# Performance work log

Measured on AMD Instinct MI355X. Metric: run time of the kernel, lower is better.

Reference implementation:

```python
import jax, jax.numpy as jnp
import numpy as np

N, E, IN_CH, H, L = 100000, 1600000, 64, 128, 4
BN_EPS = 1e-5

def setup_inputs() -> dict:
    key = jax.random.key(0)
    ks = jax.random.split(key, 20)
    s = 0.1
    return {
        'x': jax.random.normal(ks[0], (N, IN_CH), jnp.float32),
        'edge_index': jax.random.randint(ks[1], (2, E), 0, N, jnp.int64),
        'W_in': jax.random.normal(ks[2], (H, IN_CH), jnp.float32) * s,
        'b_in': jnp.zeros((H,), jnp.float32),
        'msg_W1': jax.random.normal(ks[3], (L, H, H), jnp.float32) * s,
        'msg_b1': jnp.zeros((L, H), jnp.float32),
        'msg_W2': jax.random.normal(ks[4], (L, H, H), jnp.float32) * s,
        'msg_b2': jnp.zeros((L, H), jnp.float32),
        'gru_Wih': jax.random.normal(ks[5], (L, 3 * H, H), jnp.float32) * s,
        'gru_bih': jnp.zeros((L, 3 * H), jnp.float32),
        'gru_Whh': jax.random.normal(ks[6], (L, 3 * H, H), jnp.float32) * s,
        'gru_bhh': jnp.zeros((L, 3 * H), jnp.float32),
        'bn_gamma': jnp.ones((L, H), jnp.float32),
        'bn_beta': jnp.zeros((L, H), jnp.float32),
        'W_out': jax.random.normal(ks[7], (1, H), jnp.float32) * s,
        'b_out': jnp.zeros((1,), jnp.float32),
    }

def reference(x, edge_index, W_in, b_in, msg_W1, msg_b1, msg_W2, msg_b2,
              gru_Wih, gru_bih, gru_Whh, gru_bhh, bn_gamma, bn_beta, W_out, b_out):
    n = x.shape[0]
    src, dst = edge_index[0], edge_index[1]  # j (source), i (target)
    h = jax.nn.relu(x @ W_in.T + b_in)  # [N, H]
    for l in range(L):
        residual = h
        # message: MLP on gathered source features (dropout off, eval mode)
        xj = h[src]  # [E, H] gather
        m = jax.nn.relu(xj @ msg_W1[l].T + msg_b1[l]) @ msg_W2[l].T + msg_b2[l]
        # aggregate: scatter-add into target nodes
        aggr = jax.ops.segment_sum(m, dst, num_segments=n)  # [N, H]
        # GRUCell update: input=aggr, hidden=h
        gi = aggr @ gru_Wih[l].T + gru_bih[l]  # [N, 3H]
        gh = h @ gru_Whh[l].T + gru_bhh[l]     # [N, 3H]
        i_r, i_z, i_n = jnp.split(gi, 3, axis=-1)
        h_r, h_z, h_n = jnp.split(gh, 3, axis=-1)
        r = jax.nn.sigmoid(i_r + h_r)
        z = jax.nn.sigmoid(i_z + h_z)
        ng = jnp.tanh(i_n + r * h_n)
        h = (1.0 - z) * ng + z * h
        # BatchNorm over node dim (batch statistics) + residual
        mu = jnp.mean(h, axis=0)
        var = jnp.mean((h - mu) ** 2, axis=0)
        h = bn_gamma[l] * (h - mu) * jax.lax.rsqrt(var + BN_EPS) + bn_beta[l]
        h = h + residual
    out = h @ W_out.T + b_out  # [N, 1]
    return out.squeeze(-1)
```

## Files before the change

### kernel.cpp

```cpp
#include <hip/hip_runtime.h>
#include <hip/hip_bf16.h>

#define NN 100000
#define EE 1600000
#define HH 128
#define LL 4
#define BN_EPS 1e-5f
#define NPART 6252
#define SCAN_BLK 391

typedef __attribute__((ext_vector_type(8))) short bf16x8;
typedef __attribute__((ext_vector_type(4))) float f32x4;
typedef unsigned short u16;

static __device__ __forceinline__ u16 f2bf(float f) {
  unsigned u = __float_as_uint(f);
  u += 0x7FFF + ((u >> 16) & 1);
  return (u16)(u >> 16);
}
static __device__ __forceinline__ float bf2f(u16 h) {
  return __uint_as_float(((unsigned)h) << 16);
}
static __device__ __forceinline__ void split8v(const float* v, bf16x8& hi, bf16x8& lo) {
  #pragma unroll
  for (int i = 0; i < 8; ++i) {
    u16 h = f2bf(v[i]);
    hi[i] = (short)h;
    lo[i] = (short)f2bf(v[i] - bf2f(h));
  }
}
static __device__ __forceinline__ void split8(const float* p, bf16x8& hi, bf16x8& lo) {
  float4 a = *(const float4*)p, b = *(const float4*)(p + 4);
  float v[8] = {a.x, a.y, a.z, a.w, b.x, b.y, b.z, b.w};
  split8v(v, hi, lo);
}

static __device__ __forceinline__ void gload16(const void* g, void* l) {
  __attribute__((address_space(3))) unsigned* lp =
      (__attribute__((address_space(3))) unsigned*)(reinterpret_cast<uintptr_t>(l));
  const __attribute__((address_space(1))) unsigned* gp =
      (const __attribute__((address_space(1))) unsigned*)(reinterpret_cast<uintptr_t>(g));
  __builtin_amdgcn_global_load_lds(gp, lp, 16, 0, 0);
}

__global__ void k_split(const float* __restrict__ src, u16* __restrict__ hi,
                        u16* __restrict__ lo, int n4) {
  int i = blockIdx.x * 256 + threadIdx.x;
  if (i >= n4) return;
  float4 v = ((const float4*)src)[i];
  ushort4 h_, l_;
  h_.x = f2bf(v.x); l_.x = f2bf(v.x - bf2f(h_.x));
  h_.y = f2bf(v.y); l_.y = f2bf(v.y - bf2f(h_.y));
  h_.z = f2bf(v.z); l_.z = f2bf(v.z - bf2f(h_.z));
  h_.w = f2bf(v.w); l_.w = f2bf(v.w - bf2f(h_.w));
  ((ushort4*)hi)[i] = h_;
  ((ushort4*)lo)[i] = l_;
}

__global__ void k_packsplit2(const float* __restrict__ Wff, const float* __restrict__ Whh,
                             u16* __restrict__ pW) {
  int gid = blockIdx.x * 256 + threadIdx.x;
  if (gid >= 98304) return;
  int gr = gid & 255;
  int lane = gr & 63, kk = gr >> 6;
  int rest = gid >> 8;
  int tile = rest % 12;
  int nt = (rest / 12) & 7;
  int l = rest / 96;
  int g = tile >> 2, a = tile & 3;
  int row = g * 128 + nt * 16 + (lane & 15);
  int kcol = kk * 32 + (lane >> 4) * 8;
  const float* src = ((a < 2) ? Wff : Whh) + ((size_t)l * 384 + row) * 128 + kcol;
  bf16x8 h8, l8;
  split8(src, h8, l8);
  *(bf16x8*)(pW + (size_t)gid * 8) = (a & 1) ? l8 : h8;
}

__global__ void k_idx_probe(const int* __restrict__ e32, int* __restrict__ flag) {
  if (threadIdx.x == 0 && blockIdx.x == 0) {
    int z = e32[1] | e32[3] | e32[5] | e32[7] | e32[9] | e32[11];
    flag[0] = (z == 0) ? 1 : 0;
  }
}

__global__ void k_hist(const int* __restrict__ e32, const int* __restrict__ flag,
                       int* __restrict__ degi) {
  int i = blockIdx.x * 256 + threadIdx.x;
  if (i < EE) {
    int d = flag[0] ? e32[2 * (size_t)(EE + i)] : e32[EE + i];
    atomicAdd(&degi[d], 1);
  }
}
__global__ void k_scan1(const int* __restrict__ degi, int* __restrict__ curs,
                        int* __restrict__ bsum) {
  __shared__ int s[256];
  int t = threadIdx.x;
  int i = blockIdx.x * 256 + t;
  int v = (i < NN) ? degi[i] : 0;
  s[t] = v;
  __syncthreads();
  #pragma unroll
  for (int o = 1; o < 256; o <<= 1) {
    int u = (t >= o) ? s[t - o] : 0;
    __syncthreads();
    s[t] += u;
    __syncthreads();
  }
  if (i < NN) curs[i] = s[t] - v;
  if (t == 255) bsum[blockIdx.x] = s[255];
}
__global__ void k_scan2(int* __restrict__ bsum) {
  if (threadIdx.x == 0 && blockIdx.x == 0) {
    int run = 0;
    for (int b = 0; b < SCAN_BLK; ++b) { int v = bsum[b]; bsum[b] = run; run += v; }
  }
}
__global__ void k_scan3(int* __restrict__ curs, const int* __restrict__ bsum) {
  int i = blockIdx.x * 256 + threadIdx.x;
  if (i < NN) curs[i] += bsum[blockIdx.x];
}
__global__ void k_scatter(const int* __restrict__ e32, const int* __restrict__ flag,
                          int* __restrict__ curs, int* __restrict__ es) {
  int i = blockIdx.x * 256 + threadIdx.x;
  if (i < EE) {
    int f = flag[0];
    int s = f ? e32[2 * (size_t)i] : e32[i];
    int d = f ? e32[2 * (size_t)(EE + i)] : e32[EE + i];
    int p = atomicAdd(&curs[d], 1);
    es[p] = s;
  }
}

__global__ void k_fuse_wf(const float* __restrict__ Wih, const float* __restrict__ W2,
                          float* __restrict__ Wff) {
  int li = blockIdx.x;
  int l = li / 384;
  int j = threadIdx.x;
  const float* wr = Wih + (size_t)li * 128;
  const float* w2 = W2 + (size_t)l * 128 * 128;
  float s = 0.f;
  #pragma unroll 8
  for (int k = 0; k < 128; ++k) s += wr[k] * w2[k * 128 + j];
  Wff[(size_t)li * 128 + j] = s;
}

__global__ void k_c2(const float* __restrict__ Wih, const float* __restrict__ b2,
                     float* __restrict__ c2) {
  int gid = blockIdx.x * 256 + threadIdx.x;
  if (gid >= 4 * 384) return;
  int l = gid / 384;
  const float* wr = Wih + (size_t)gid * 128;
  const float* br = b2 + (size_t)l * 128;
  float s = 0.f;
  #pragma unroll 8
  for (int k = 0; k < 128; ++k) s += wr[k] * br[k];
  c2[gid] = s;
}

__global__ __launch_bounds__(256) void k_inproj2(
    const float* __restrict__ x, const float* __restrict__ Win,
    const float* __restrict__ bin, float* __restrict__ hf) {
  __shared__ u16 xh[64][72], xl[64][72];
  const int t = threadIdx.x;
  const int wv = t >> 6, ln = t & 63;
  const int lr = ln & 15, lg = ln >> 4;
  const int nb = blockIdx.x * 64;

  #pragma unroll
  for (int it = 0; it < 4; ++it) {
    int idx = t + it * 256;
    int row = idx >> 4, c4 = idx & 15;
    int node = nb + row;
    float4 v = (node < NN) ? ((const float4*)(x + (size_t)node * 64))[c4]
                           : make_float4(0.f, 0.f, 0.f, 0.f);
    ushort4 h_, l_;
    h_.x = f2bf(v.x); l_.x = f2bf(v.x - bf2f(h_.x));
    h_.y = f2bf(v.y); l_.y = f2bf(v.y - bf2f(h_.y));
    h_.z = f2bf(v.z); l_.z = f2bf(v.z - bf2f(h_.z));
    h_.w = f2bf(v.w); l_.w = f2bf(v.w - bf2f(h_.w));
    *(ushort4*)&xh[row][c4 * 4] = h_;
    *(ushort4*)&xl[row][c4 * 4] = l_;
  }
  __syncthreads();

  f32x4 acc[4][2];
  #pragma unroll
  for (int rt = 0; rt < 4; ++rt)
    #pragma unroll
    for (int nt = 0; nt < 2; ++nt)
      acc[rt][nt] = (f32x4){0.f, 0.f, 0.f, 0.f};

  bf16x8 bh[2][2], bl[2][2];
  #pragma unroll
  for (int nt = 0; nt < 2; ++nt) {
    int c = wv * 32 + nt * 16 + lr;
    #pragma unroll
    for (int kk = 0; kk < 2; ++kk)
      split8(Win + (size_t)c * 64 + kk * 32 + lg * 8, bh[nt][kk], bl[nt][kk]);
  }

  #pragma unroll
  for (int rt = 0; rt < 4; ++rt) {
    bf16x8 ah[2], al[2];
    #pragma unroll
    for (int kk = 0; kk < 2; ++kk) {
      ah[kk] = *(const bf16x8*)(&xh[rt * 16 + lr][kk * 32 + lg * 8]);
      al[kk] = *(const bf16x8*)(&xl[rt * 16 + lr][kk * 32 + lg * 8]);
    }
    #pragma unroll
    for (int nt = 0; nt < 2; ++nt) {
      #pragma unroll
      for (int kk = 0; kk < 2; ++kk) {
        acc[rt][nt] = __builtin_amdgcn_mfma_f32_16x16x32_bf16(ah[kk], bh[nt][kk], acc[rt][nt], 0, 0, 0);
        acc[rt][nt] = __builtin_amdgcn_mfma_f32_16x16x32_bf16(ah[kk], bl[nt][kk], acc[rt][nt], 0, 0, 0);
        acc[rt][nt] = __builtin_amdgcn_mfma_f32_16x16x32_bf16(al[kk], bh[nt][kk], acc[rt][nt], 0, 0, 0);
      }
    }
  }

  #pragma unroll
  for (int nt = 0; nt < 2; ++nt) {
    int col = wv * 32 + nt * 16 + lr;
    float bias = bin[col];
    #pragma unroll
    for (int rt = 0; rt < 4; ++rt) {
      #pragma unroll
      for (int r = 0; r < 4; ++r) {
        int node = nb + rt * 16 + lg * 4 + r;
        if (node < NN)
          hf[(size_t)node * 128 + col] = fmaxf(acc[rt][nt][r] + bias, 0.f);
      }
    }
  }
}

__global__ __launch_bounds__(256) void k_relu1(
    const float* __restrict__ hgru, const float* __restrict__ bnsc,
    const float* __restrict__ bnsh, const float* __restrict__ hf_in,
    float* __restrict__ hf_out,
    const u16* __restrict__ W1h, const u16* __restrict__ W1l,
    const float* __restrict__ b1, float* __restrict__ R, int fuse_bn) {
  __shared__ bf16x8 ghx[1024], glx[1024];
  const int t = threadIdx.x;
  const int wv = t >> 6, ln = t & 63;
  const int lr = ln & 15, lg = ln >> 4;
  const int nb = blockIdx.x * 64;

  #pragma unroll
  for (int rt = 0; rt < 4; ++rt) {
    int row = nb + rt * 16 + (ln & 15);
    int rc = min(row, NN - 1);
    int kcol = wv * 32 + (ln >> 4) * 8;
    const float* hp = hf_in + (size_t)rc * 128 + kcol;
    float v[8];
    if (fuse_bn) {
      const float* gp = hgru + (size_t)rc * 128 + kcol;
      float4 g0 = *(const float4*)gp, g1 = *(const float4*)(gp + 4);
      float4 h0 = *(const float4*)hp, h1 = *(const float4*)(hp + 4);
      float4 sc0 = *(const float4*)(bnsc + kcol), sc1 = *(const float4*)(bnsc + kcol + 4);
      float4 sh0 = *(const float4*)(bnsh + kcol), sh1 = *(const float4*)(bnsh + kcol + 4);
      v[0] = g0.x * sc0.x + sh0.x + h0.x;
      v[1] = g0.y * sc0.y + sh0.y + h0.y;
      v[2] = g0.z * sc0.z + sh0.z + h0.z;
      v[3] = g0.w * sc0.w + sh0.w + h0.w;
      v[4] = g1.x * sc1.x + sh1.x + h1.x;
      v[5] = g1.y * sc1.y + sh1.y + h1.y;
      v[6] = g1.z * sc1.z + sh1.z + h1.z;
      v[7] = g1.w * sc1.w + sh1.w + h1.w;
      if (row < NN) {
        float* op = hf_out + (size_t)row * 128 + kcol;
        *(float4*)op = make_float4(v[0], v[1], v[2], v[3]);
        *(float4*)(op + 4) = make_float4(v[4], v[5], v[6], v[7]);
      }
    } else {
      float4 h0 = *(const float4*)hp, h1 = *(const float4*)(hp + 4);
      v[0] = h0.x; v[1] = h0.y; v[2] = h0.z; v[3] = h0.w;
      v[4] = h1.x; v[5] = h1.y; v[6] = h1.z; v[7] = h1.w;
    }
    bf16x8 h8, l8;
    split8v(v, h8, l8);
    ghx[rt * 256 + t] = h8;
    glx[rt * 256 + t] = l8;
  }
  __syncthreads();

  bf16x8 bh[2][4], bl[2][4];
  #pragma unroll
  for (int nt = 0; nt < 2; ++nt) {
    size_t wb = (size_t)(wv * 32 + nt * 16 + lr) * 128 + lg * 8;
    #pragma unroll
    for (int kk = 0; kk < 4; ++kk) {
      bh[nt][kk] = *(const bf16x8*)(W1h + wb + kk * 32);
      bl[nt][kk] = *(const bf16x8*)(W1l + wb + kk * 32);
    }
  }

  f32x4 acc[4][2];
  #pragma unroll
  for (int rt = 0; rt < 4; ++rt)
    #pragma unroll
    for (int nt = 0; nt < 2; ++nt)
      acc[rt][nt] = (f32x4){0.f, 0.f, 0.f, 0.f};

  #pragma unroll
  for (int rt = 0; rt < 4; ++rt) {
    bf16x8 ah[4], al[4];
    #pragma unroll
    for (int kk = 0; kk < 4; ++kk) {
      ah[kk] = ghx[(rt * 4 + kk) * 64 + ln];
      al[kk] = glx[(rt * 4 + kk) * 64 + ln];
    }
    #pragma unroll
    for (int nt = 0; nt < 2; ++nt) {
      #pragma unroll
      for (int kk = 0; kk < 4; ++kk) {
        acc[rt][nt] = __builtin_amdgcn_mfma_f32_16x16x32_bf16(ah[kk], bh[nt][kk], acc[rt][nt], 0, 0, 0);
        acc[rt][nt] = __builtin_amdgcn_mfma_f32_16x16x32_bf16(ah[kk], bl[nt][kk], acc[rt][nt], 0, 0, 0);
        acc[rt][nt] = __builtin_amdgcn_mfma_f32_16x16x32_bf16(al[kk], bh[nt][kk], acc[rt][nt], 0, 0, 0);
      }
    }
  }

  #pragma unroll
  for (int nt = 0; nt < 2; ++nt) {
    int col = wv * 32 + nt * 16 + lr;
    float bias = b1[col];
    #pragma unroll
    for (int rt = 0; rt < 4; ++rt) {
      #pragma unroll
      for (int r = 0; r < 4; ++r) {
        int node = nb + rt * 16 + lg * 4 + r;
        if (node < NN)
          R[(size_t)node * 128 + col] = fmaxf(acc[rt][nt][r] + bias, 0.f);
      }
    }
  }
}

__global__ __launch_bounds__(256) void k_aggr(
    const float* __restrict__ R, const int* __restrict__ es,
    const int* __restrict__ rowend, float* __restrict__ aggr) {
  const int t = threadIdx.x;
  const int node = blockIdx.x * 4 + (t >> 6);
  const int cp = (t & 63) * 2;
  if (node >= NN) return;
  const int k0 = (node == 0) ? 0 : rowend[node - 1];
  const int k1 = rowend[node];
  float sx0 = 0.f, sx1 = 0.f, sx2 = 0.f, sx3 = 0.f;
  float sy0 = 0.f, sy1 = 0.f, sy2 = 0.f, sy3 = 0.f;
  int k = k0;
  for (; k + 4 <= k1; k += 4) {
    int e0 = es[k], e1 = es[k + 1], e2 = es[k + 2], e3 = es[k + 3];
    float2 v0 = *(const float2*)(R + (size_t)e0 * 128 + cp);
    float2 v1 = *(const float2*)(R + (size_t)e1 * 128 + cp);
    float2 v2 = *(const float2*)(R + (size_t)e2 * 128 + cp);
    float2 v3 = *(const float2*)(R + (size_t)e3 * 128 + cp);
    sx0 += v0.x; sy0 += v0.y;
    sx1 += v1.x; sy1 += v1.y;
    sx2 += v2.x; sy2 += v2.y;
    sx3 += v3.x; sy3 += v3.y;
  }
  for (; k < k1; ++k) {
    float2 v = *(const float2*)(R + (size_t)es[k] * 128 + cp);
    sx0 += v.x; sy0 += v.y;
  }
  size_t o = (size_t)node * 128 + cp;
  aggr[o] = (sx0 + sx1) + (sx2 + sx3);
  aggr[o + 1] = (sy0 + sy1) + (sy2 + sy3);
}

#define MFMA3(ACC, AH, AL, BH, BL)                                             \
  ACC = __builtin_amdgcn_mfma_f32_16x16x32_bf16(AH, BH, ACC, 0, 0, 0);         \
  ACC = __builtin_amdgcn_mfma_f32_16x16x32_bf16(AH, BL, ACC, 0, 0, 0);         \
  ACC = __builtin_amdgcn_mfma_f32_16x16x32_bf16(AL, BH, ACC, 0, 0, 0);

__global__ __launch_bounds__(256) void k_gru(
    const float* __restrict__ aggr, const float* __restrict__ hf,
    const u16* __restrict__ pW,
    const float* __restrict__ c2, const float* __restrict__ bih,
    const float* __restrict__ bhh, const int* __restrict__ degi,
    float* __restrict__ hgru, double* __restrict__ partials) {
  __shared__ uint4 wlds4[12 * 256];
  u16* wlds = (u16*)wlds4;
  const int t = threadIdx.x;
  const int ln = t & 63, wv = t >> 6;
  const int lr = ln & 15, lg = ln >> 4;
  const int nb = blockIdx.x * 64 + wv * 16;
  const int rowc = min(nb + lr, NN - 1);
  const size_t prow = ((size_t)blockIdx.x * 4 + wv) * 256;

  bf16x8 Aah[4], Aal[4], Ahh[4], Ahl[4];
  #pragma unroll
  for (int kk = 0; kk < 4; ++kk) {
    int c0 = kk * 32 + lg * 8;
    split8(aggr + (size_t)rowc * 128 + c0, Aah[kk], Aal[kk]);
    split8(hf + (size_t)rowc * 128 + c0, Ahh[kk], Ahl[kk]);
  }

  float degs[4];
  int noderow[4];
  #pragma unroll
  for (int r = 0; r < 4; ++r) {
    noderow[r] = min(nb + lg * 4 + r, NN - 1);
    degs[r] = (float)degi[noderow[r]];
  }

  #pragma unroll 1
  for (int nt = 0; nt < 8; ++nt) {
    const int col = nt * 16 + lr;

    float fh[4];
    #pragma unroll
    for (int r = 0; r < 4; ++r)
      fh[r] = hf[(size_t)noderow[r] * 128 + col];

    __syncthreads();
    #pragma unroll
    for (int j = 0; j < 12; ++j) {
      size_t gidx = (size_t)nt * 3072 + j * 256 + t;
      gload16(pW + gidx * 8, wlds + (size_t)(j * 256 + t) * 8);
    }
    __syncthreads();

    f32x4 ar = (f32x4){0.f, 0.f, 0.f, 0.f};
    f32x4 az = ar, ai = ar, an = ar;
    #pragma unroll
    for (int kk = 0; kk < 4; ++kk) {
      const bf16x8* wb = (const bf16x8*)wlds + kk * 64 + ln;
      bf16x8 brh = wb[0 * 256];
      bf16x8 brl = wb[1 * 256];
      bf16x8 crh = wb[2 * 256];
      bf16x8 crl = wb[3 * 256];
      MFMA3(ar, Aah[kk], Aal[kk], brh, brl)
      MFMA3(ar, Ahh[kk], Ahl[kk], crh, crl)
      bf16x8 bzh = wb[4 * 256];
      bf16x8 bzl = wb[5 * 256];
      bf16x8 czh = wb[6 * 256];
      bf16x8 czl = wb[7 * 256];
      MFMA3(az, Aah[kk], Aal[kk], bzh, bzl)
      MFMA3(az, Ahh[kk], Ahl[kk], czh, czl)
      bf16x8 bnh = wb[8 * 256];
      bf16x8 bnl = wb[9 * 256];
      bf16x8 cnh = wb[10 * 256];
      bf16x8 cnl = wb[11 * 256];
      MFMA3(ai, Aah[kk], Aal[kk], bnh, bnl)
      MFMA3(an, Ahh[kk], Ahl[kk], cnh, cnl)
    }

    float c2r = c2[col], c2z = c2[128 + col], c2n = c2[256 + col];
    float br = bih[col] + bhh[col];
    float bz = bih[128 + col] + bhh[128 + col];
    float bin_ = bih[256 + col], bhn = bhh[256 + col];
    double s = 0.0, s2 = 0.0;
    #pragma unroll
    for (int r = 0; r < 4; ++r) {
      int node = nb + lg * 4 + r;
      bool valid = node < NN;
      float d = degs[r];
      float sr = ar[r] + d * c2r + br;
      float sz = az[r] + d * c2z + bz;
      float rg = 1.f / (1.f + __expf(-sr));
      float zg = 1.f / (1.f + __expf(-sz));
      float ngin = ai[r] + d * c2n + bin_ + rg * (an[r] + bhn);
      float e2 = __expf(-2.f * fabsf(ngin));
      float ng = __builtin_copysignf((1.f - e2) / (1.f + e2), ngin);
      float hn = (1.f - zg) * ng + zg * fh[r];
      if (valid) {
        hgru[(size_t)node * 128 + col] = hn;
        s += (double)hn;
        s2 += (double)hn * (double)hn;
      }
    }
    s += __shfl_xor(s, 16);  s += __shfl_xor(s, 32);
    s2 += __shfl_xor(s2, 16); s2 += __shfl_xor(s2, 32);
    if (lg == 0) {
      partials[prow + col] = s;
      partials[prow + 128 + col] = s2;
    }
  }
}

__global__ void k_bnred_a(const double* __restrict__ partials, double* __restrict__ interm) {
  int b = blockIdx.x;
  int c = threadIdx.x;
  double s = 0.0;
  int i0 = b * 98, i1 = min(i0 + 98, NPART);
  for (int i = i0; i < i1; ++i) s += partials[(size_t)i * 256 + c];
  interm[b * 256 + c] = s;
}
__global__ void k_bnred_b(const double* __restrict__ interm, const float* __restrict__ gamma,
                          const float* __restrict__ beta, float* __restrict__ bnsc,
                          float* __restrict__ bnsh) {
  int c = threadIdx.x;
  double s = 0.0, s2 = 0.0;
  for (int i = 0; i < 64; ++i) {
    s += interm[i * 256 + c];
    s2 += interm[i * 256 + 128 + c];
  }
  double mu = s / (double)NN;
  double var = s2 / (double)NN - mu * mu;
  float sc = (float)((double)gamma[c] / sqrt(var + (double)BN_EPS));
  bnsc[c] = sc;
  bnsh[c] = (float)((double)beta[c] - mu * (double)sc);
}

__global__ void k_bnapply(const float* __restrict__ hgru, const float* __restrict__ bnsc,
                          const float* __restrict__ bnsh, float* __restrict__ hf) {
  int i = blockIdx.x * 256 + threadIdx.x;
  int c4 = i & 31;
  float4 g = ((const float4*)hgru)[i];
  float4 sc = ((const float4*)bnsc)[c4];
  float4 sh = ((const float4*)bnsh)[c4];
  float4 h = ((const float4*)hf)[i];
  float4 o;
  o.x = g.x * sc.x + sh.x + h.x;
  o.y = g.y * sc.y + sh.y + h.y;
  o.z = g.z * sc.z + sh.z + h.z;
  o.w = g.w * sc.w + sh.w + h.w;
  ((float4*)hf)[i] = o;
}

__global__ void k_out(const float* __restrict__ hf, const float* __restrict__ wout,
                      const float* __restrict__ bout, float* __restrict__ out) {
  int ln = threadIdx.x & 63;
  int n = blockIdx.x * 4 + (threadIdx.x >> 6);
  float2 w = ((const float2*)wout)[ln];
  float2 v = ((const float2*)(hf + (size_t)n * 128))[ln];
  float s = v.x * w.x + v.y * w.y;
  #pragma unroll
  for (int d = 32; d > 0; d >>= 1) s += __shfl_xor(s, d);
  if (ln == 0) out[n] = s + bout[0];
}

extern "C" void kernel_launch(void* const* d_in, const int* in_sizes, int n_in,
                              void* d_out, int out_size, void* d_ws, size_t ws_size,
                              hipStream_t stream) {
  const float* x = (const float*)d_in[0];
  const int* eraw = (const int*)d_in[1];
  const float* Win = (const float*)d_in[2];
  const float* bin = (const float*)d_in[3];
  const float* mW1 = (const float*)d_in[4];
  const float* mb1 = (const float*)d_in[5];
  const float* mW2 = (const float*)d_in[6];
  const float* mb2 = (const float*)d_in[7];
  const float* Wih = (const float*)d_in[8];
  const float* bih = (const float*)d_in[9];
  const float* Whh = (const float*)d_in[10];
  const float* bhh = (const float*)d_in[11];
  const float* gamma = (const float*)d_in[12];
  const float* beta = (const float*)d_in[13];
  const float* wout = (const float*)d_in[14];
  const float* bout = (const float*)d_in[15];
  float* out = (float*)d_out;

  char* ws = (char*)d_ws;
  size_t off = 0;
  auto carve = [&](size_t b) -> char* {
    char* p = ws + off;
    off = (off + b + 255) & ~(size_t)255;
    return p;
  };
  float* Hbuf0 = (float*)carve(sizeof(float) * NN * HH);
  float* Hbuf1 = (float*)carve(sizeof(float) * NN * HH);
  float* RG0 = (float*)carve(sizeof(float) * NN * HH);
  float* RG1 = (float*)carve(sizeof(float) * NN * HH);
  int* es = (int*)carve(sizeof(int) * EE);
  int* idxflag = (int*)carve(sizeof(int) * 64);
  int* degi = (int*)carve(sizeof(int) * NN);
  int* curs = (int*)carve(sizeof(int) * NN);
  int* bsum = (int*)carve(sizeof(int) * SCAN_BLK);
  double* partials = (double*)carve(sizeof(double) * NPART * 256);
  double* interm = (double*)carve(sizeof(double) * 64 * 256);
  float* bnsc = (float*)carve(sizeof(float) * 128);
  float* bnsh = (float*)carve(sizeof(float) * 128);
  u16* W1h = (u16*)carve(sizeof(u16) * 4 * HH * HH);
  u16* W1l = (u16*)carve(sizeof(u16) * 4 * HH * HH);
  float* Wff = (float*)carve(sizeof(float) * 4 * 384 * HH);
  u16* pW = (u16*)carve(sizeof(u16) * 4 * 24576 * 8);
  float* c2 = (float*)carve(sizeof(float) * 4 * 384);

  float* Hbuf[2] = {Hbuf0, Hbuf1};
  float* RG[2] = {RG0, RG1};

  k_idx_probe<<<1, 64, 0, stream>>>(eraw, idxflag);

  hipMemsetAsync(degi, 0, sizeof(int) * NN, stream);
  k_hist<<<(EE + 255) / 256, 256, 0, stream>>>(eraw, idxflag, degi);
  k_scan1<<<SCAN_BLK, 256, 0, stream>>>(degi, curs, bsum);
  k_scan2<<<1, 64, 0, stream>>>(bsum);
  k_scan3<<<SCAN_BLK, 256, 0, stream>>>(curs, bsum);
  k_scatter<<<(EE + 255) / 256, 256, 0, stream>>>(eraw, idxflag, curs, es);

  k_split<<<(4 * HH * HH / 4) / 256, 256, 0, stream>>>(mW1, W1h, W1l, 4 * HH * HH / 4);
  k_fuse_wf<<<4 * 384, 128, 0, stream>>>(Wih, mW2, Wff);
  k_packsplit2<<<384, 256, 0, stream>>>(Wff, Whh, pW);
  k_c2<<<6, 256, 0, stream>>>(Wih, mb2, c2);

  k_inproj2<<<(NN + 63) / 64, 256, 0, stream>>>(x, Win, bin, Hbuf[0]);

  for (int l = 0; l < LL; ++l) {
    const float* h_old = Hbuf[(l == 0) ? 0 : ((l - 1) & 1)];
    float* h_cur = Hbuf[l & 1];
    float* Rbuf = RG[l & 1];
    const float* hgru_prev = RG[(l == 0) ? 1 : ((l - 1) & 1)];
    float* aggr = Hbuf[(l + 1) & 1];
    k_relu1<<<(NN + 63) / 64, 256, 0, stream>>>(
        hgru_prev, bnsc, bnsh, h_old, h_cur,
        W1h + (size_t)l * HH * HH, W1l + (size_t)l * HH * HH,
        mb1 + l * HH, Rbuf, l > 0 ? 1 : 0);
    k_aggr<<<(NN + 3) / 4, 256, 0, stream>>>(Rbuf, es, curs, aggr);
    k_gru<<<(NN + 63) / 64, 256, 0, stream>>>(
        aggr, h_cur, pW + (size_t)l * 24576 * 8,
        c2 + l * 384, bih + l * 384, bhh + l * 384, degi, Rbuf , partials);
    k_bnred_a<<<64, 256, 0, stream>>>(partials, interm);
    k_bnred_b<<<1, 128, 0, stream>>>(interm, gamma + l * HH, beta + l * HH, bnsc, bnsh);
  }
  k_bnapply<<<(NN * HH / 4) / 256, 256, 0, stream>>>(RG[(LL - 1) & 1], bnsc, bnsh,
                                                     Hbuf[(LL - 1) & 1]);
  k_out<<<NN / 4, 256, 0, stream>>>(Hbuf[(LL - 1) & 1], wout, bout, out);
}
```

Baseline: 1.509 ms.

## Fuse CSR neighbor aggregation into GRU kernel via shared-memory staging

Drops the separate aggregation kernel. Each wave of the GRU kernel now gathers and sums the neighbor messages for its 16 nodes, stages them in a shared-memory tile that shares a union with the weight buffer, and reads its MFMA A-operands from there. This removes the write and re-read of the N×128 aggr buffer and one launch per layer. The cost is that each wave walks 16 nodes serially with only 64 lanes, so gather parallelism and latency hiding inside the GRU kernel may be lower. The hgru output now goes to the other RG buffer instead of overwriting R.

```diff
diff --git a/kernel.cpp b/kernel.cpp
--- a/kernel.cpp
+++ b/kernel.cpp
@@ -239,7 +239,7 @@
     const float* __restrict__ bnsh, const float* __restrict__ hf_in,
     float* __restrict__ hf_out,
     const u16* __restrict__ W1h, const u16* __restrict__ W1l,
-    const float* __restrict__ b1, float* __restrict__ R, int fuse_bn) {
+    const float* __restrict__ b1, float* R, int fuse_bn) {
   __shared__ bf16x8 ghx[1024], glx[1024];
   const int t = threadIdx.x;
   const int wv = t >> 6, ln = t & 63;
@@ -337,51 +337,24 @@
   }
 }
 
-__global__ __launch_bounds__(256) void k_aggr(
-    const float* __restrict__ R, const int* __restrict__ es,
-    const int* __restrict__ rowend, float* __restrict__ aggr) {
-  const int t = threadIdx.x;
-  const int node = blockIdx.x * 4 + (t >> 6);
-  const int cp = (t & 63) * 2;
-  if (node >= NN) return;
-  const int k0 = (node == 0) ? 0 : rowend[node - 1];
-  const int k1 = rowend[node];
-  float sx0 = 0.f, sx1 = 0.f, sx2 = 0.f, sx3 = 0.f;
-  float sy0 = 0.f, sy1 = 0.f, sy2 = 0.f, sy3 = 0.f;
-  int k = k0;
-  for (; k + 4 <= k1; k += 4) {
-    int e0 = es[k], e1 = es[k + 1], e2 = es[k + 2], e3 = es[k + 3];
-    float2 v0 = *(const float2*)(R + (size_t)e0 * 128 + cp);
-    float2 v1 = *(const float2*)(R + (size_t)e1 * 128 + cp);
-    float2 v2 = *(const float2*)(R + (size_t)e2 * 128 + cp);
-    float2 v3 = *(const float2*)(R + (size_t)e3 * 128 + cp);
-    sx0 += v0.x; sy0 += v0.y;
-    sx1 += v1.x; sy1 += v1.y;
-    sx2 += v2.x; sy2 += v2.y;
-    sx3 += v3.x; sy3 += v3.y;
-  }
-  for (; k < k1; ++k) {
-    float2 v = *(const float2*)(R + (size_t)es[k] * 128 + cp);
-    sx0 += v.x; sy0 += v.y;
-  }
-  size_t o = (size_t)node * 128 + cp;
-  aggr[o] = (sx0 + sx1) + (sx2 + sx3);
-  aggr[o + 1] = (sy0 + sy1) + (sy2 + sy3);
-}
-
 #define MFMA3(ACC, AH, AL, BH, BL)                                             \
   ACC = __builtin_amdgcn_mfma_f32_16x16x32_bf16(AH, BH, ACC, 0, 0, 0);         \
   ACC = __builtin_amdgcn_mfma_f32_16x16x32_bf16(AH, BL, ACC, 0, 0, 0);         \
   ACC = __builtin_amdgcn_mfma_f32_16x16x32_bf16(AL, BH, ACC, 0, 0, 0);
 
 __global__ __launch_bounds__(256) void k_gru(
-    const float* __restrict__ aggr, const float* __restrict__ hf,
+    const float* __restrict__ R, const float* __restrict__ hf,
+    const int* __restrict__ es, const int* __restrict__ rowend,
     const u16* __restrict__ pW,
     const float* __restrict__ c2, const float* __restrict__ bih,
     const float* __restrict__ bhh, const int* __restrict__ degi,
     float* __restrict__ hgru, double* __restrict__ partials) {
-  __shared__ uint4 wlds4[12 * 256];
-  u16* wlds = (u16*)wlds4;
+  union SM {
+    float aggT[4][16][132];
+    uint4 w[12 * 256];
+  };
+  __shared__ SM sm;
+  u16* wlds = (u16*)sm.w;
   const int t = threadIdx.x;
   const int ln = t & 63, wv = t >> 6;
   const int lr = ln & 15, lg = ln >> 4;
@@ -389,11 +362,44 @@
   const int rowc = min(nb + lr, NN - 1);
   const size_t prow = ((size_t)blockIdx.x * 4 + wv) * 256;
 
+  {
+    const int cp = ln * 2;
+    #pragma unroll 1
+    for (int i = 0; i < 16; ++i) {
+      int nc = min(nb + i, NN - 1);
+      int k0 = (nc == 0) ? 0 : rowend[nc - 1];
+      int k1 = rowend[nc];
+      float sx0 = 0.f, sx1 = 0.f, sx2 = 0.f, sx3 = 0.f;
+      float sy0 = 0.f, sy1 = 0.f, sy2 = 0.f, sy3 = 0.f;
+      int k = k0;
+      for (; k + 4 <= k1; k += 4) {
+        int e0 = es[k], e1 = es[k + 1], e2 = es[k + 2], e3 = es[k + 3];
+        float2 v0 = *(const float2*)(R + (size_t)e0 * 128 + cp);
+        float2 v1 = *(const float2*)(R + (size_t)e1 * 128 + cp);
+        float2 v2 = *(const float2*)(R + (size_t)e2 * 128 + cp);
+        float2 v3 = *(const float2*)(R + (size_t)e3 * 128 + cp);
+        sx0 += v0.x; sy0 += v0.y;
+        sx1 += v1.x; sy1 += v1.y;
+        sx2 += v2.x; sy2 += v2.y;
+        sx3 += v3.x; sy3 += v3.y;
+      }
+      for (; k < k1; ++k) {
+        float2 v = *(const float2*)(R + (size_t)es[k] * 128 + cp);
+        sx0 += v.x; sy0 += v.y;
+      }
+      sm.aggT[wv][i][cp] = (sx0 + sx1) + (sx2 + sx3);
+      sm.aggT[wv][i][cp + 1] = (sy0 + sy1) + (sy2 + sy3);
+    }
+  }
+
   bf16x8 Aah[4], Aal[4], Ahh[4], Ahl[4];
   #pragma unroll
   for (int kk = 0; kk < 4; ++kk) {
     int c0 = kk * 32 + lg * 8;
-    split8(aggr + (size_t)rowc * 128 + c0, Aah[kk], Aal[kk]);
+    float v[8];
+    #pragma unroll
+    for (int j = 0; j < 8; ++j) v[j] = sm.aggT[wv][lr][c0 + j];
+    split8v(v, Aah[kk], Aal[kk]);
     split8(hf + (size_t)rowc * 128 + c0, Ahh[kk], Ahl[kk]);
   }
 
@@ -602,20 +608,19 @@
     const float* h_old = Hbuf[(l == 0) ? 0 : ((l - 1) & 1)];
     float* h_cur = Hbuf[l & 1];
     float* Rbuf = RG[l & 1];
-    const float* hgru_prev = RG[(l == 0) ? 1 : ((l - 1) & 1)];
-    float* aggr = Hbuf[(l + 1) & 1];
+    const float* hgru_prev = RG[l & 1];
+    float* hgru_cur = RG[(l + 1) & 1];
     k_relu1<<<(NN + 63) / 64, 256, 0, stream>>>(
         hgru_prev, bnsc, bnsh, h_old, h_cur,
         W1h + (size_t)l * HH * HH, W1l + (size_t)l * HH * HH,
         mb1 + l * HH, Rbuf, l > 0 ? 1 : 0);
-    k_aggr<<<(NN + 3) / 4, 256, 0, stream>>>(Rbuf, es, curs, aggr);
     k_gru<<<(NN + 63) / 64, 256, 0, stream>>>(
-        aggr, h_cur, pW + (size_t)l * 24576 * 8,
-        c2 + l * 384, bih + l * 384, bhh + l * 384, degi, Rbuf , partials);
+        Rbuf, h_cur, es, curs, pW + (size_t)l * 24576 * 8,
+        c2 + l * 384, bih + l * 384, bhh + l * 384, degi, hgru_cur, partials);
     k_bnred_a<<<64, 256, 0, stream>>>(partials, interm);
     k_bnred_b<<<1, 128, 0, stream>>>(interm, gamma + l * HH, beta + l * HH, bnsc, bnsh);
   }
-  k_bnapply<<<(NN * HH / 4) / 256, 256, 0, stream>>>(RG[(LL - 1) & 1], bnsc, bnsh,
+  k_bnapply<<<(NN * HH / 4) / 256, 256, 0, stream>>>(RG[LL & 1], bnsc, bnsh,
                                                      Hbuf[(LL - 1) & 1]);
   k_out<<<NN / 4, 256, 0, stream>>>(Hbuf[(LL - 1) & 1], wout, bout, out);
 }
```

Result: slower. 1.909 ms (+26.5%).
